# Performance work log

Hardware: AMD Instinct MI355X
Metric: run time of the kernel (lower is better)

Reference implementation:

```python
import jax, jax.numpy as jnp
import numpy as np

S, B, C, H, W = 16, 64, 128, 11, 11
P = H * W
N_ITER = 3
EPS = 1e-5


def setup_inputs() -> dict:
    key = jax.random.key(0)
    ks = jax.random.split(key, 12)
    w = lambda k, shape: jax.random.normal(k, shape, jnp.float32) * 0.02
    return {
        "x": jax.random.normal(ks[0], (S, B, C, H, W), jnp.float32),
        # intra-attention 1x1 convs (stored as [out,in] matrices)
        "wq": w(ks[1], (C, C)), "bq": jnp.zeros((C,), jnp.float32),
        "wk": w(ks[2], (C, C)), "bk": jnp.zeros((C,), jnp.float32),
        "wv": w(ks[3], (C, C)), "bv": jnp.zeros((C,), jnp.float32),
        "intra_alpha": jnp.float32(1.0),
        # inter-message path
        "w_msg": w(ks[4], (C, C + 1)), "b_msg": jnp.zeros((C,), jnp.float32),
        "w_lin": w(ks[5], (C, C)),
        "weight": jnp.float32(0.5),
        "w_gate": w(ks[6], (C, C)), "b_gate": jnp.zeros((C,), jnp.float32),
        # ConvGRU 3x3 convs
        "w_zr": w(ks[7], (2 * C, 2 * C, 3, 3)), "b_zr": jnp.zeros((2 * C,), jnp.float32),
        "w_h": w(ks[8], (C, 2 * C, 3, 3)), "b_h": jnp.zeros((C,), jnp.float32),
        # LayerNorm over [C,11,11]
        "ln_gamma": jnp.ones((C, H, W), jnp.float32),
        "ln_beta": jnp.zeros((C, H, W), jnp.float32),
    }


def reference(x, wq, bq, wk, bk, wv, bv, intra_alpha, w_msg, b_msg, w_lin,
              weight, w_gate, b_gate, w_zr, b_zr, w_h, b_h, ln_gamma, ln_beta):
    scale = C ** -0.5

    def c1(t, wgt, bias):  # 1x1 conv on [S,B,Cin,H,W] -> [S,B,Cout,H,W]
        return jnp.einsum('sbchw,oc->sbohw', t, wgt) + bias[:, None, None]

    def conv3(t, wgt, bias):  # 3x3 'SAME' conv on [N,Cin,H,W]
        y = jax.lax.conv_general_dilated(
            t, wgt, (1, 1), 'SAME', dimension_numbers=('NCHW', 'OIHW', 'NCHW'))
        return y + bias[None, :, None, None]

    # chain-graph neighbor validity masks (|i-j| == 1)
    mask_l = (jnp.arange(S) >= 1).astype(x.dtype)[:, None, None, None, None]
    mask_r = (jnp.arange(S) <= S - 2).astype(x.dtype)[:, None, None, None, None]

    h = x
    for _ in range(N_ITER):
        # ---- intra spatial self-attention (per node, over P=H*W tokens) ----
        q = c1(h, wq, bq).reshape(S, B, C, P)
        k = c1(h, wk, bk).reshape(S, B, C, P)
        v = c1(h, wv, bv).reshape(S, B, C, P)
        att = jax.nn.softmax(jnp.einsum('sbcp,sbcq->sbpq', q, k) * scale, axis=-1)
        intra = jnp.einsum('sbpq,sbcq->sbcp', att, v).reshape(S, B, C, H, W)
        intra = intra_alpha * intra + h

        # ---- inter gated message attention from chain neighbors ----
        xf = h.reshape(S, B, C, P)

        def gated_msg(y, edge_val):
            ef = jnp.full((S, B, 1, H, W), edge_val, h.dtype)  # edge feature i-j
            yy = c1(jnp.concatenate([y, ef], axis=2), w_msg, b_msg).reshape(S, B, C, P)
            yy = jnp.einsum('sbcp,dc->sbdp', yy, w_lin)  # Linear (no bias)
            a = jax.nn.softmax(jnp.einsum('sbcp,sbcq->sbpq', xf, yy), axis=-1)
            m = jnp.einsum('sbpq,sbcq->sbcp', a, yy).reshape(S, B, C, H, W)
            g = jax.nn.sigmoid(c1(m, w_gate, b_gate).mean(axis=(-2, -1), keepdims=True))
            return m * g

        y_left = jnp.concatenate([jnp.zeros_like(h[:1]), h[:-1]], axis=0)   # h[i-1], edge +1
        y_right = jnp.concatenate([h[1:], jnp.zeros_like(h[:1])], axis=0)   # h[i+1], edge -1
        inter = gated_msg(y_left, 1.0) * mask_l + gated_msg(y_right, -1.0) * mask_r

        comb = weight * intra + (1.0 - weight) * inter

        # ---- ConvGRU update (fold S into batch) ----
        xg = comb.reshape(S * B, C, H, W)
        hg = h.reshape(S * B, C, H, W)
        zr = jax.nn.sigmoid(conv3(jnp.concatenate([xg, hg], axis=1), w_zr, b_zr))
        z, r = zr[:, :C], zr[:, C:]
        h_hat = jnp.tanh(conv3(jnp.concatenate([xg, r * hg], axis=1), w_h, b_h))
        h_new = ((1 - z) * hg + z * h_hat).reshape(S, B, C, H, W)

        # ---- residual + LayerNorm over [C,H,W] ----
        nh = h_new + h
        mu = nh.mean(axis=(-3, -2, -1), keepdims=True)
        var = nh.var(axis=(-3, -2, -1), keepdims=True)
        h = (nh - mu) * jax.lax.rsqrt(var + EPS) * ln_gamma + ln_beta
    return h
```

## Files before the change

### kernel.cpp

```cpp
#include <hip/hip_runtime.h>
#include <hip/hip_bf16.h>

#define S_   16
#define B_   64
#define SBn  1024
#define C_   128
#define P_   121
#define CP_  15488
static const long NEl = 15859712L;

typedef __hip_bfloat16 bf16t;
typedef __attribute__((ext_vector_type(8))) short bf16x8;
typedef __attribute__((ext_vector_type(4))) float f32x4;
typedef __attribute__((ext_vector_type(4))) unsigned short us4;

__device__ __forceinline__ float ldb(const bf16t* p){ return __bfloat162float(*p); }
__device__ __forceinline__ float b2f(unsigned short u){ unsigned x=((unsigned)u)<<16; float f; __builtin_memcpy(&f,&x,4); return f; }
__device__ __forceinline__ unsigned short f2bu(float v){ __hip_bfloat16 b=__float2bfloat16(v); unsigned short u; __builtin_memcpy(&u,&b,2); return u; }
__device__ __forceinline__ float ldin(const void* s, long i, int f){
    return f ? ((const float*)s)[i] : b2f(((const unsigned short*)s)[i]);
}

__global__ void detect_kernel(const unsigned short* __restrict__ x, int* __restrict__ flag){
    if(blockIdx.x==0 && threadIdx.x==0){
        int crazy=0;
        for(int i=0;i<512;i++){
            unsigned e=(x[i]>>7)&0xFF;
            if(e!=0 && (e<64 || e>191)) crazy++;
        }
        *flag=(crazy>40)?1:0;
    }
}

__global__ void cvt_kernel(float* __restrict__ dst, const void* __restrict__ src, long n, const int* __restrict__ flag){
    long i=(long)blockIdx.x*blockDim.x+threadIdx.x;
    long st=(long)gridDim.x*blockDim.x;
    int f=*flag;
    for(;i<n;i+=st) dst[i]=ldin(src,i,f);
}

__global__ __launch_bounds__(256) void cvtT_kernel(bf16t* __restrict__ hT, const void* __restrict__ x, const int* __restrict__ flag){
    __shared__ bf16t tl[CP_];
    int sb=blockIdx.x, t=threadIdx.x; int f=*flag;
    for(int i=t;i<CP_;i+=256)
        tl[i]=__float2bfloat16(ldin(x,(long)sb*CP_+i,f));
    __syncthreads();
    bf16t* ho=hT+(size_t)sb*CP_;
    for(int j=t;j<CP_;j+=256){
        int p=j>>7, c=j&127;
        ho[j]=tl[c*P_+p];
    }
}

__global__ __launch_bounds__(128) void prep_msg_kernel(float* __restrict__ W2, float* __restrict__ b2l, float* __restrict__ b2r,
        const void* __restrict__ wlin, const void* __restrict__ wmsg, const void* __restrict__ bmsg, const int* __restrict__ flag){
    int d=blockIdx.x, c=threadIdx.x; int f=*flag;
    float acc=0.f;
    for(int o2=0;o2<C_;o2++) acc += ldin(wlin,(long)d*C_+o2,f)*ldin(wmsg,(long)o2*(C_+1)+c,f);
    W2[d*C_+c]=acc;
    if(c<2){
        float e=(c==0)?1.f:-1.f; float a=0.f;
        for(int o2=0;o2<C_;o2++) a += ldin(wlin,(long)d*C_+o2,f)*(ldin(bmsg,o2,f)+e*ldin(wmsg,(long)o2*(C_+1)+C_,f));
        if(c==0) b2l[d]=a; else b2r[d]=a;
    }
}

template<int RAW>
__global__ void prep_w1t(bf16t* __restrict__ dst, const void* __restrict__ src, const int* __restrict__ flag){
    int idx=blockIdx.x*blockDim.x+threadIdx.x;
    if(idx>=16384) return;
    int r=idx&31, oc=(idx>>5)&127, icb=idx>>12;
    float v = RAW? ldin(src,(long)oc*C_+icb*32+r,*flag) : ((const float*)src)[(long)oc*C_+icb*32+r];
    dst[idx]=__float2bfloat16(v);
}

__global__ void prep_w3t(bf16t* __restrict__ dst, const void* __restrict__ src, const int* __restrict__ flag, int OC){
    int idx=blockIdx.x*blockDim.x+threadIdx.x;
    int tot=OC*2304;
    if(idx>=tot) return;
    int r=idx&31; int rest=idx>>5; int oc=rest%OC; int g2=rest/OC; int icb=g2&7, tap=g2>>3;
    float v=ldin(src,((long)(oc*256+icb*32+r))*9+tap,*flag);
    dst[idx]=__float2bfloat16(v);
}

__global__ void prep_gbt(float* __restrict__ gamT, float* __restrict__ betT,
                         const void* __restrict__ gam, const void* __restrict__ bet, const int* __restrict__ flag){
    int idx=blockIdx.x*blockDim.x+threadIdx.x;
    if(idx>=CP_) return;
    int c=idx/P_, p=idx-c*P_; int f=*flag;
    gamT[p*C_+c]=ldin(gam,idx,f);
    betT[p*C_+c]=ldin(bet,idx,f);
}

__global__ void prep_wgt(float* __restrict__ wgT, float* __restrict__ bg2,
                         const void* __restrict__ wg, const void* __restrict__ bg, const int* __restrict__ flag){
    int idx=blockIdx.x*blockDim.x+threadIdx.x;
    int f=*flag;
    if(idx<16384){ int k=idx>>7, c=idx&127; wgT[idx]=ldin(wg,(long)c*C_+k,f); }
    if(idx<128) bg2[idx]=ldin(bg,idx,f);
}

__device__ __forceinline__ void gemm24r(f32x4 (&acc)[4][2],
    const bf16t* __restrict__ Wt, const bf16x8 (&hreg)[4][2],
    int ocr,int l15,int kg)
{
    #pragma unroll
    for(int i=0;i<4;i++){
        #pragma unroll
        for(int j=0;j<2;j++) acc[i][j]=(f32x4){0.f,0.f,0.f,0.f};
    }
    #pragma unroll
    for(int kc=0;kc<4;kc++){
        bf16x8 a[4];
        #pragma unroll
        for(int mt=0;mt<4;mt++) a[mt]=*(const bf16x8*)(Wt+((size_t)(kc*C_+ocr*64+mt*16+l15))*32+kg*8);
        #pragma unroll
        for(int mt=0;mt<4;mt++){
            #pragma unroll
            for(int nt=0;nt<2;nt++)
                acc[mt][nt]=__builtin_amdgcn_mfma_f32_16x16x32_bf16(a[mt],hreg[kc][nt],acc[mt][nt],0,0,0);
        }
    }
}

__global__ __launch_bounds__(512) void qkv_attn(
    bf16t* __restrict__ comb, const bf16t* __restrict__ hT,
    const bf16t* __restrict__ WqT, const bf16t* __restrict__ WkT, const bf16t* __restrict__ WvT,
    const float* __restrict__ bq, const float* __restrict__ bk, const float* __restrict__ bv,
    const float* __restrict__ alphap, const float* __restrict__ wp)
{
    __shared__ bf16t LA[128*136];
    __shared__ bf16t LB[128*136];
    int sb=blockIdx.x, t=threadIdx.x, lane=t&63, w=t>>6;
    int l15=lane&15, kg=lane>>4;
    const bf16t* hp=hT+(size_t)sb*CP_;
    int ocr=w>>2, pcr=w&3;
    bf16x8 hreg[4][2];
    #pragma unroll
    for(int kc=0;kc<4;kc++){
        #pragma unroll
        for(int nt=0;nt<2;nt++)
            hreg[kc][nt]=*(const bf16x8*)(hp+(size_t)(pcr*32+nt*16+l15)*C_+kc*32+kg*8);
    }
    f32x4 acc[4][2];
    gemm24r(acc,WqT,hreg,ocr,l15,kg);
    #pragma unroll
    for(int mt=0;mt<4;mt++){
        int oc0=ocr*64+mt*16+kg*4;
        #pragma unroll
        for(int nt=0;nt<2;nt++){
            int p=pcr*32+nt*16+l15;
            us4 pk;
            #pragma unroll
            for(int r=0;r<4;r++) pk[r]=f2bu(acc[mt][nt][r]+bq[oc0+r]);
            *(us4*)(LA+p*136+oc0)=pk;
        }
    }
    gemm24r(acc,WkT,hreg,ocr,l15,kg);
    #pragma unroll
    for(int mt=0;mt<4;mt++){
        int oc0=ocr*64+mt*16+kg*4;
        #pragma unroll
        for(int nt=0;nt<2;nt++){
            int p=pcr*32+nt*16+l15;
            us4 pk;
            #pragma unroll
            for(int r=0;r<4;r++) pk[r]=f2bu(acc[mt][nt][r]+bk[oc0+r]);
            *(us4*)(LB+p*136+oc0)=pk;
        }
    }
    __syncthreads();
    int m0=w*16;
    f32x4 s[8];
    #pragma unroll
    for(int nt=0;nt<8;nt++) s[nt]=(f32x4){0.f,0.f,0.f,0.f};
    #pragma unroll
    for(int kc=0;kc<4;kc++){
        bf16x8 a=*(const bf16x8*)(LA+(size_t)(m0+l15)*136+kc*32+kg*8);
        #pragma unroll
        for(int nt=0;nt<8;nt++){
            bf16x8 b=*(const bf16x8*)(LB+(size_t)(nt*16+l15)*136+kc*32+kg*8);
            s[nt]=__builtin_amdgcn_mfma_f32_16x16x32_bf16(a,b,s[nt],0,0,0);
        }
    }
    const float scale=0.08838834764831845f;
    #pragma unroll
    for(int nt=0;nt<8;nt++){
        #pragma unroll
        for(int r=0;r<4;r++) s[nt][r]*=scale;
    }
    if(l15>=9){
        #pragma unroll
        for(int r=0;r<4;r++) s[7][r]=-3.0e38f;
    }
    #pragma unroll
    for(int r=0;r<4;r++){
        float mx=s[0][r];
        #pragma unroll
        for(int nt=1;nt<8;nt++) mx=fmaxf(mx,s[nt][r]);
        #pragma unroll
        for(int o=1;o<16;o<<=1) mx=fmaxf(mx,__shfl_xor(mx,o));
        float sm=0.f;
        #pragma unroll
        for(int nt=0;nt<8;nt++){ float e=__expf(s[nt][r]-mx); s[nt][r]=e; sm+=e; }
        #pragma unroll
        for(int o=1;o<16;o<<=1) sm+=__shfl_xor(sm,o);
        float rs=1.f/sm;
        #pragma unroll
        for(int nt=0;nt<8;nt++) s[nt][r]*=rs;
    }
    __syncthreads();
    gemm24r(acc,WvT,hreg,ocr,l15,kg);
    #pragma unroll
    for(int mt=0;mt<4;mt++){
        int oc0=ocr*64+mt*16+kg*4;
        #pragma unroll
        for(int nt=0;nt<2;nt++){
            int p=pcr*32+nt*16+l15;
            #pragma unroll
            for(int r=0;r<4;r++)
                LA[(oc0+r)*136+p]=__float2bfloat16(p<P_? acc[mt][nt][r]+bv[oc0+r] : 0.f);
        }
    }
    #pragma unroll
    for(int r=0;r<4;r++){
        int pr=m0+kg*4+r;
        #pragma unroll
        for(int nt=0;nt<8;nt++) LB[pr*136+nt*16+l15]=__float2bfloat16(s[nt][r]);
    }
    __syncthreads();
    f32x4 o[8];
    #pragma unroll
    for(int nt=0;nt<8;nt++) o[nt]=(f32x4){0.f,0.f,0.f,0.f};
    #pragma unroll
    for(int jc=0;jc<4;jc++){
        bf16x8 a=*(const bf16x8*)(LA+(size_t)(m0+l15)*136+jc*32+kg*8);
        #pragma unroll
        for(int nt=0;nt<8;nt++){
            bf16x8 b=*(const bf16x8*)(LB+(size_t)(nt*16+l15)*136+jc*32+kg*8);
            o[nt]=__builtin_amdgcn_mfma_f32_16x16x32_bf16(a,b,o[nt],0,0,0);
        }
    }
    float al=*alphap, wv=*wp;
    int c0=m0+kg*4;
    bf16t* ob=comb+(size_t)sb*CP_;
    #pragma unroll
    for(int nt=0;nt<8;nt++){
        int p=nt*16+l15;
        if(p>=P_) continue;
        us4 hv=*(const us4*)(hp+(size_t)p*C_+c0);
        us4 pk;
        #pragma unroll
        for(int r=0;r<4;r++) pk[r]=f2bu(wv*(al*o[nt][r]+b2f(hv[r])));
        *(us4*)(ob+(size_t)p*C_+c0)=pk;
    }
}

__global__ __launch_bounds__(512) void msg_all(
    bf16t* __restrict__ comb, const bf16t* __restrict__ hT,
    const bf16t* __restrict__ W2T, const float* __restrict__ b2e,
    const float* __restrict__ wgT, const float* __restrict__ bgf,
    const float* __restrict__ wp, int sb0, int shift)
{
    __shared__ bf16t LA[128*136];
    __shared__ bf16t LB[128*136];
    __shared__ float fl[256];
    int sb=sb0+blockIdx.x, t=threadIdx.x, lane=t&63, w=t>>6;
    int l15=lane&15, kg=lane>>4;
    const bf16t* hsp=hT+(size_t)(sb+shift)*CP_;
    int ocr=w>>2, pcr=w&3;
    bf16x8 hreg[4][2];
    #pragma unroll
    for(int kc=0;kc<4;kc++){
        #pragma unroll
        for(int nt=0;nt<2;nt++)
            hreg[kc][nt]=*(const bf16x8*)(hsp+(size_t)(pcr*32+nt*16+l15)*C_+kc*32+kg*8);
    }
    f32x4 acc[4][2];
    gemm24r(acc,W2T,hreg,ocr,l15,kg);
    #pragma unroll
    for(int mt=0;mt<4;mt++){
        int oc0=ocr*64+mt*16+kg*4;
        #pragma unroll
        for(int nt=0;nt<2;nt++){
            int p=pcr*32+nt*16+l15;
            us4 pk;
            #pragma unroll
            for(int r=0;r<4;r++){
                float v=acc[mt][nt][r]+b2e[oc0+r];
                pk[r]=f2bu(v);
                LB[(oc0+r)*136+p]=__float2bfloat16(p<P_? v : 0.f);
            }
            *(us4*)(LA+p*136+oc0)=pk;
        }
    }
    __syncthreads();
    int m0=w*16;
    const bf16t* ap=hT+(size_t)sb*CP_;
    f32x4 s[8];
    #pragma unroll
    for(int nt=0;nt<8;nt++) s[nt]=(f32x4){0.f,0.f,0.f,0.f};
    #pragma unroll
    for(int kc=0;kc<4;kc++){
        bf16x8 a=*(const bf16x8*)(ap+(size_t)(m0+l15)*C_+kc*32+kg*8);
        #pragma unroll
        for(int nt=0;nt<8;nt++){
            bf16x8 b=*(const bf16x8*)(LA+(size_t)(nt*16+l15)*136+kc*32+kg*8);
            s[nt]=__builtin_amdgcn_mfma_f32_16x16x32_bf16(a,b,s[nt],0,0,0);
        }
    }
    if(l15>=9){
        #pragma unroll
        for(int r=0;r<4;r++) s[7][r]=-3.0e38f;
    }
    #pragma unroll
    for(int r=0;r<4;r++){
        float mx=s[0][r];
        #pragma unroll
        for(int nt=1;nt<8;nt++) mx=fmaxf(mx,s[nt][r]);
        #pragma unroll
        for(int o=1;o<16;o<<=1) mx=fmaxf(mx,__shfl_xor(mx,o));
        float sm=0.f;
        #pragma unroll
        for(int nt=0;nt<8;nt++){ float e=__expf(s[nt][r]-mx); s[nt][r]=e; sm+=e; }
        #pragma unroll
        for(int o=1;o<16;o<<=1) sm+=__shfl_xor(sm,o);
        float rs=1.f/sm;
        #pragma unroll
        for(int nt=0;nt<8;nt++) s[nt][r]*=rs;
    }
    __syncthreads();
    #pragma unroll
    for(int r=0;r<4;r++){
        int pr=m0+kg*4+r;
        #pragma unroll
        for(int nt=0;nt<8;nt++) LA[pr*136+nt*16+l15]=__float2bfloat16(s[nt][r]);
    }
    __syncthreads();
    f32x4 o[8];
    #pragma unroll
    for(int nt=0;nt<8;nt++) o[nt]=(f32x4){0.f,0.f,0.f,0.f};
    #pragma unroll
    for(int jc=0;jc<4;jc++){
        bf16x8 a=*(const bf16x8*)(LB+(size_t)(m0+l15)*136+jc*32+kg*8);
        #pragma unroll
        for(int nt=0;nt<8;nt++){
            bf16x8 b=*(const bf16x8*)(LA+(size_t)(nt*16+l15)*136+jc*32+kg*8);
            o[nt]=__builtin_amdgcn_mfma_f32_16x16x32_bf16(a,b,o[nt],0,0,0);
        }
    }
    int c0=m0+kg*4;
    #pragma unroll
    for(int r=0;r<4;r++){
        float sm=0.f;
        #pragma unroll
        for(int nt=0;nt<8;nt++){ float v=o[nt][r]; if(nt==7&&l15>8) v=0.f; sm+=v; }
        sm+=__shfl_xor(sm,1); sm+=__shfl_xor(sm,2); sm+=__shfl_xor(sm,4); sm+=__shfl_xor(sm,8);
        if(l15==0) fl[c0+r]=sm*(1.f/121.f);
    }
    __syncthreads();
    if(t<C_){
        float a=bgf[t];
        #pragma unroll 8
        for(int k=0;k<C_;k++) a+=wgT[k*C_+t]*fl[k];
        fl[C_+t]=1.f/(1.f+__expf(-a));
    }
    __syncthreads();
    float w1m=1.f-*wp;
    float gg[4];
    #pragma unroll
    for(int r=0;r<4;r++) gg[r]=fl[C_+c0+r];
    bf16t* ob=comb+(size_t)sb*CP_;
    #pragma unroll
    for(int nt=0;nt<8;nt++){
        int p=nt*16+l15;
        if(p>=P_) continue;
        us4 bv=*(const us4*)(ob+(size_t)p*C_+c0);
        #pragma unroll
        for(int r=0;r<4;r++) bv[r]=f2bu(b2f(bv[r]) + w1m*o[nt][r]*gg[r]);
        *(us4*)(ob+(size_t)p*C_+c0)=bv;
    }
}

#define LOADA3(bidx, widx) { \
    _Pragma("unroll") \
    for(int mt=0;mt<4;mt++) abuf[bidx][mt]=*(const bf16x8*)(Wt+(size_t)(widx)*(OC*32)+mt*512+base_lane); }
#define STEP3(lbase, bidx, doff) { \
    bf16x8 bb[4]; \
    _Pragma("unroll") \
    for(int nt=0;nt<4;nt++) bb[nt]=*(const bf16x8*)((lbase)+boff[nt]+(doff)); \
    __builtin_amdgcn_s_setprio(1); \
    _Pragma("unroll") \
    for(int mt=0;mt<4;mt++){ \
        _Pragma("unroll") \
        for(int nt=0;nt<4;nt++) \
            acc[mt][nt]=__builtin_amdgcn_mfma_f32_16x16x32_bf16(abuf[bidx][mt],bb[nt],acc[mt][nt],0,0,0); } \
    __builtin_amdgcn_s_setprio(0); }

#define SLOADZ(stg) { \
    const bf16t* ssrc=(((stg)<2)? in0T:in1T)+(size_t)sb*CP_+((stg)&1)*64; \
    sreg[0]=*(const bf16x8*)(ssrc+(size_t)sp0*C_+(t&7)*8); \
    if(sv1) sreg[1]=*(const bf16x8*)(ssrc+(size_t)sp1*C_+(t&7)*8); }
#define SWRITEZ(lbase) { \
    *(bf16x8*)((lbase)+spix0*72+(t&7)*8)=sreg[0]; \
    if(sv1) *(bf16x8*)((lbase)+spix1*72+(t&7)*8)=sreg[1]; }

__global__ __launch_bounds__(512) void conv3_zr(
    bf16t* __restrict__ o0, bf16t* __restrict__ o1,
    const bf16t* __restrict__ in0T, const bf16t* __restrict__ in1T,
    const bf16t* __restrict__ Wt, const float* __restrict__ bias,
    const bf16t* __restrict__ hTb)
{
    constexpr int OC=256;
    __shared__ bf16t lin[2*12176];
    int sb=blockIdx.x;
    int t=threadIdx.x, lane=t&63, w=t>>6;
    int ocb=(w>=4)?128:0; int w2=w&3;
    int ocr=w2>>1, pcr=w2&1, l15=lane&15, kg=lane>>4;
    int boff[4]; bool pv_[4];
    #pragma unroll
    for(int nt=0;nt<4;nt++){
        int p=pcr*64+nt*16+l15;
        pv_[nt]=(p<P_); int pc=pv_[nt]?p:(P_-1);
        boff[nt]=((pc/11)*13+(pc%11))*72+kg*8;
    }
    f32x4 acc[4][4];
    #pragma unroll
    for(int i=0;i<4;i++){
        #pragma unroll
        for(int j=0;j<4;j++) acc[i][j]=(f32x4){0.f,0.f,0.f,0.f};
    }
    int base_lane=(ocb+ocr*64+l15)*32+kg*8;
    bf16x8 abuf[4][4];
    bf16x8 sreg[2];
    bool sv1=((t+512)<968);
    int sp0=t>>3, sp1=(t+512)>>3;
    if(sp1>120) sp1=120;
    int spix0=(sp0/11+1)*13+(sp0%11)+1;
    int spix1=(sp1/11+1)*13+(sp1%11)+1;
    LOADA3(0,0); LOADA3(1,1); LOADA3(2,8); LOADA3(3,9);
    SLOADZ(0);
    {
        bf16x8 z;
        #pragma unroll
        for(int e=0;e<8;e++) z[e]=0;
        for(int i=t;i<768;i+=512){
            int half=i>=384; int i2=i-half*384;
            int bi=i2>>3, cc=(i2&7)*8;
            int pix;
            if(bi<13) pix=bi;
            else if(bi<26) pix=156+(bi-13);
            else { int j2=bi-26; pix=(1+(j2>>1))*13+((j2&1)?12:0); }
            *(bf16x8*)(lin+half*12176+pix*72+cc)=z;
        }
    }
    SWRITEZ(lin);
    __syncthreads();
    #pragma unroll
    for(int st=0; st<4; ++st){
        if(st<3) SLOADZ(st+1);
        bf16t* lbase=lin+(st&1)*12176;
        #pragma unroll
        for(int k=0;k<18;k++){
            int s=st*18+k;
            int tap=k>>1, l=k&1;
            int doff=((tap/3)*13+(tap%3))*72+l*32;
            STEP3(lbase, s&3, doff);
            if(s<68){
                int s4=s+4, st4=s4/18, k4=s4-st4*18, tap4=k4>>1, l4=k4&1;
                LOADA3(s&3, tap4*8+st4*2+l4);
            }
        }
        if(st<3){ SWRITEZ(lin+((st+1)&1)*12176); }
        __syncthreads();
    }
    #pragma unroll
    for(int mt=0;mt<4;mt++){
        int ocl=ocr*64+mt*16+kg*4;
        #pragma unroll
        for(int nt=0;nt<4;nt++){
            if(!pv_[nt]) continue;
            int p=pcr*64+nt*16+l15;
            size_t tb=(size_t)sb*CP_+(size_t)p*C_+ocl;
            us4 pk;
            if(ocb==0){
                #pragma unroll
                for(int r=0;r<4;r++){ float a=acc[mt][nt][r]+bias[ocl+r]; pk[r]=f2bu(1.f/(1.f+__expf(-a))); }
                *(us4*)(o0+tb)=pk;
            }else{
                us4 hv=*(const us4*)(hTb+tb);
                #pragma unroll
                for(int r=0;r<4;r++){ float a=acc[mt][nt][r]+bias[128+ocl+r]; float sg=1.f/(1.f+__expf(-a)); pk[r]=f2bu(sg*b2f(hv[r])); }
                *(us4*)(o1+tb)=pk;
            }
        }
    }
}

#define SLOADH(stg) { \
    const bf16t* ssrc=(((stg)<2)? in0T:in1T)+(size_t)sb*CP_+((stg)&1)*64; \
    sreg[0]=*(const bf16x8*)(ssrc+(size_t)(t>>3)*C_+(t&7)*8); \
    sreg[1]=*(const bf16x8*)(ssrc+(size_t)((t+256)>>3)*C_+(t&7)*8); \
    if(sv2) sreg[2]=*(const bf16x8*)(ssrc+(size_t)sp2*C_+(t&7)*8); \
    if(sv3) sreg[3]=*(const bf16x8*)(ssrc+(size_t)sp3*C_+(t&7)*8); }
#define SWRITEH(lbase) { \
    *(bf16x8*)((lbase)+spix0*72+(t&7)*8)=sreg[0]; \
    *(bf16x8*)((lbase)+spix1*72+(t&7)*8)=sreg[1]; \
    if(sv2) *(bf16x8*)((lbase)+spix2*72+(t&7)*8)=sreg[2]; \
    if(sv3) *(bf16x8*)((lbase)+spix3*72+(t&7)*8)=sreg[3]; }

__global__ __launch_bounds__(256) void conv3_hh(
    bf16t* __restrict__ o0,
    const bf16t* __restrict__ in0T, const bf16t* __restrict__ in1T,
    const bf16t* __restrict__ Wt, const float* __restrict__ bias,
    const bf16t* __restrict__ zT, const bf16t* __restrict__ hTb,
    const float* __restrict__ gamT, const float* __restrict__ betT)
{
    constexpr int OC=128;
    __shared__ bf16t lin[2*12176];
    __shared__ float red[8];
    int sb=blockIdx.x;
    int t=threadIdx.x, lane=t&63, w=t>>6;
    int ocr=w>>1, pcr=w&1, l15=lane&15, kg=lane>>4;
    int boff[4]; bool pv_[4];
    #pragma unroll
    for(int nt=0;nt<4;nt++){
        int p=pcr*64+nt*16+l15;
        pv_[nt]=(p<P_); int pc=pv_[nt]?p:(P_-1);
        boff[nt]=((pc/11)*13+(pc%11))*72+kg*8;
    }
    f32x4 acc[4][4];
    #pragma unroll
    for(int i=0;i<4;i++){
        #pragma unroll
        for(int j=0;j<4;j++) acc[i][j]=(f32x4){0.f,0.f,0.f,0.f};
    }
    int base_lane=(ocr*64+l15)*32+kg*8;
    bf16x8 abuf[4][4];
    bf16x8 sreg[4];
    bool sv2=((t+512)<968), sv3=((t+768)<968);
    int sp0=t>>3, sp1=(t+256)>>3, sp2=(t+512)>>3, sp3=(t+768)>>3;
    if(sp2>120) sp2=120;
    if(sp3>120) sp3=120;
    int spix0=(sp0/11+1)*13+(sp0%11)+1;
    int spix1=(sp1/11+1)*13+(sp1%11)+1;
    int spix2=(sp2/11+1)*13+(sp2%11)+1;
    int spix3=(sp3/11+1)*13+(sp3%11)+1;
    LOADA3(0,0); LOADA3(1,1); LOADA3(2,8); LOADA3(3,9);
    SLOADH(0);
    {
        bf16x8 z;
        #pragma unroll
        for(int e=0;e<8;e++) z[e]=0;
        for(int i=t;i<768;i+=256){
            int half=i>=384; int i2=i-half*384;
            int bi=i2>>3, cc=(i2&7)*8;
            int pix;
            if(bi<13) pix=bi;
            else if(bi<26) pix=156+(bi-13);
            else { int j2=bi-26; pix=(1+(j2>>1))*13+((j2&1)?12:0); }
            *(bf16x8*)(lin+half*12176+pix*72+cc)=z;
        }
    }
    SWRITEH(lin);
    __syncthreads();
    #pragma unroll
    for(int st=0; st<4; ++st){
        if(st<3) SLOADH(st+1);
        bf16t* lbase=lin+(st&1)*12176;
        #pragma unroll
        for(int k=0;k<18;k++){
            int s=st*18+k;
            int tap=k>>1, l=k&1;
            int doff=((tap/3)*13+(tap%3))*72+l*32;
            STEP3(lbase, s&3, doff);
            if(s<68){
                int s4=s+4, st4=s4/18, k4=s4-st4*18, tap4=k4>>1, l4=k4&1;
                LOADA3(s&3, tap4*8+st4*2+l4);
            }
        }
        if(st<3){ SWRITEH(lin+((st+1)&1)*12176); }
        __syncthreads();
    }
    float ls=0.f, ls2=0.f;
    #pragma unroll
    for(int mt=0;mt<4;mt++){
        int ocl=ocr*64+mt*16+kg*4;
        #pragma unroll
        for(int nt=0;nt<4;nt++){
            if(!pv_[nt]) continue;
            int p=pcr*64+nt*16+l15;
            size_t tb=(size_t)sb*CP_+(size_t)p*C_+ocl;
            us4 hv=*(const us4*)(hTb+tb);
            us4 zv=*(const us4*)(zT+tb);
            us4 pk;
            #pragma unroll
            for(int r=0;r<4;r++){
                float a=acc[mt][nt][r]+bias[ocl+r];
                float ht=tanhf(a);
                float z=b2f(zv[r]), h=b2f(hv[r]);
                unsigned short u=f2bu((1.f-z)*h+z*ht+h);
                pk[r]=u;
                float nr=b2f(u); ls+=nr; ls2+=nr*nr;
            }
            *(us4*)((unsigned short*)lin + p*C_+ocl)=pk;
        }
    }
    #pragma unroll
    for(int o=32;o;o>>=1){ ls+=__shfl_xor(ls,o); ls2+=__shfl_xor(ls2,o); }
    if(lane==0){ red[w]=ls; red[4+w]=ls2; }
    __syncthreads();
    float Sx=red[0]+red[1]+red[2]+red[3];
    float Sx2=red[4]+red[5]+red[6]+red[7];
    float mu=Sx*(1.f/(float)CP_);
    float var=Sx2*(1.f/(float)CP_)-mu*mu;
    float rstd=rsqrtf(var+1e-5f);
    bf16t* ho=o0+(size_t)sb*CP_;
    for(int i=t;i<CP_;i+=256){
        float v=(ldb(lin+i)-mu)*rstd*gamT[i]+betT[i];
        ho[i]=__float2bfloat16(v);
    }
}

__global__ __launch_bounds__(256) void finalT_kernel(void* __restrict__ fout, const bf16t* __restrict__ hT, const int* __restrict__ flag){
    __shared__ bf16t tl[CP_];
    int sb=blockIdx.x, t=threadIdx.x, f=*flag;
    for(int i=t;i<CP_;i+=256) tl[i]=hT[(size_t)sb*CP_+i];
    __syncthreads();
    for(int i=t;i<CP_;i+=256){
        int c=i/P_, p=i-c*P_;
        float v=ldb(tl+p*C_+c);
        size_t oi=(size_t)sb*CP_+i;
        if(f) ((float*)fout)[oi]=v;
        else  ((bf16t*)fout)[oi]=__float2bfloat16(v);
    }
}

extern "C" void kernel_launch(void* const* d_in, const int* in_sizes, int n_in,
                              void* d_out, int out_size, void* d_ws, size_t ws_size,
                              hipStream_t stream) {
    (void)in_sizes; (void)n_in; (void)out_size;
    char* base=(char*)d_ws;
    size_t off=0;
    auto alloc=[&](size_t bytes){ void* p=base+off; off+=(bytes+255)&~(size_t)255; return p; };
    bf16t* b1=(bf16t*)alloc((size_t)NEl*2+8192);
    bf16t* b2=(bf16t*)alloc((size_t)NEl*2+8192);
    bf16t* b3=(bf16t*)alloc((size_t)NEl*2+8192);
    bf16t* b4=(bf16t*)d_out;
    bf16t* wqT=(bf16t*)alloc(16384*2);
    bf16t* wkT=(bf16t*)alloc(16384*2);
    bf16t* wvT=(bf16t*)alloc(16384*2);
    bf16t* w2T=(bf16t*)alloc(16384*2);
    bf16t* wzrT=(bf16t*)alloc((size_t)589824*2);
    bf16t* whT =(bf16t*)alloc((size_t)294912*2);
    float* W2f=(float*)alloc(16384*4);
    float* b2l=(float*)alloc(128*4); float* b2r=(float*)alloc(128*4);
    float* bqf=(float*)alloc(128*4); float* bkf=(float*)alloc(128*4); float* bvf=(float*)alloc(128*4);
    float* bzrf=(float*)alloc(256*4); float* bhf=(float*)alloc(128*4);
    float* gamT=(float*)alloc(15488*4); float* betT=(float*)alloc(15488*4);
    float* wgTf=(float*)alloc(16384*4); float* bgf2=(float*)alloc(128*4);
    float* alphaf=(float*)alloc(4); float* weightf=(float*)alloc(4);
    int* flag=(int*)alloc(4);
    if(ws_size<off) return;

    detect_kernel<<<1,64,0,stream>>>((const unsigned short*)d_in[0],flag);
    cvtT_kernel<<<SBn,256,0,stream>>>(b1,d_in[0],flag);
    prep_w1t<1><<<64,256,0,stream>>>(wqT,d_in[1],flag);
    cvt_kernel<<<1,128,0,stream>>>(bqf,d_in[2],128,flag);
    prep_w1t<1><<<64,256,0,stream>>>(wkT,d_in[3],flag);
    cvt_kernel<<<1,128,0,stream>>>(bkf,d_in[4],128,flag);
    prep_w1t<1><<<64,256,0,stream>>>(wvT,d_in[5],flag);
    cvt_kernel<<<1,128,0,stream>>>(bvf,d_in[6],128,flag);
    cvt_kernel<<<1,64,0,stream>>>(alphaf,d_in[7],1,flag);
    prep_msg_kernel<<<C_,C_,0,stream>>>(W2f,b2l,b2r,d_in[10],d_in[8],d_in[9],flag);
    prep_w1t<0><<<64,256,0,stream>>>(w2T,W2f,flag);
    cvt_kernel<<<1,64,0,stream>>>(weightf,d_in[11],1,flag);
    prep_wgt<<<64,256,0,stream>>>(wgTf,bgf2,d_in[12],d_in[13],flag);
    prep_w3t<<<(256*2304+255)/256,256,0,stream>>>(wzrT,d_in[14],flag,256);
    cvt_kernel<<<1,256,0,stream>>>(bzrf,d_in[15],256,flag);
    prep_w3t<<<(128*2304+255)/256,256,0,stream>>>(whT,d_in[16],flag,128);
    cvt_kernel<<<1,128,0,stream>>>(bhf,d_in[17],128,flag);
    prep_gbt<<<(CP_+255)/256,256,0,stream>>>(gamT,betT,d_in[18],d_in[19],flag);

    for(int it=0; it<3; ++it){
        qkv_attn<<<SBn,512,0,stream>>>(b2,b1,wqT,wkT,wvT,bqf,bkf,bvf,alphaf,weightf);
        msg_all<<<SBn-B_,512,0,stream>>>(b2,b1,w2T,b2l,wgTf,bgf2,weightf,B_,-B_);
        msg_all<<<SBn-B_,512,0,stream>>>(b2,b1,w2T,b2r,wgTf,bgf2,weightf,0,B_);
        conv3_zr<<<SBn,512,0,stream>>>(b4,b3,b2,b1,wzrT,bzrf,b1);
        conv3_hh<<<SBn,256,0,stream>>>(b1,b2,b3,whT,bhf,b4,b1,gamT,betT);
    }
    finalT_kernel<<<SBn,256,0,stream>>>(d_out,b1,flag);
}
```

Measured before the change: 1.424 ms.

## Fuse intra-attention and both inter-message kernels into one per-node kernel

Merges qkv_attn and the two msg_all launches into a single attn_all kernel that keeps the combined result in registers and writes comb once. This removes two launches per iteration and the read-modify-write round trips of comb through global memory. It also reuses the node's own h tile (areg) across both message phases. The cost is higher register pressure (res, areg and hreg all live at once), which may reduce occupancy, and each block now does its message phases serially instead of spreading them over separate launches.

```diff
diff --git a/kernel.cpp b/kernel.cpp
--- a/kernel.cpp
+++ b/kernel.cpp
@@ -123,161 +123,25 @@
     }
 }
 
-__global__ __launch_bounds__(512) void qkv_attn(
-    bf16t* __restrict__ comb, const bf16t* __restrict__ hT,
-    const bf16t* __restrict__ WqT, const bf16t* __restrict__ WkT, const bf16t* __restrict__ WvT,
-    const float* __restrict__ bq, const float* __restrict__ bk, const float* __restrict__ bv,
-    const float* __restrict__ alphap, const float* __restrict__ wp)
+__device__ __forceinline__ void msg_phase(
+    f32x4 (&res)[8], const bf16t* __restrict__ hT, int sb, int shift,
+    const bf16t* __restrict__ W2T, const float* __restrict__ b2e,
+    const float* __restrict__ wgT, const float* __restrict__ bgf, float w1m,
+    const bf16x8 (&areg)[4],
+    bf16t* LA, bf16t* LB, float* fl,
+    int t,int w,int l15,int kg,int ocr,int pcr)
 {
-    __shared__ bf16t LA[128*136];
-    __shared__ bf16t LB[128*136];
-    int sb=blockIdx.x, t=threadIdx.x, lane=t&63, w=t>>6;
-    int l15=lane&15, kg=lane>>4;
-    const bf16t* hp=hT+(size_t)sb*CP_;
-    int ocr=w>>2, pcr=w&3;
-    bf16x8 hreg[4][2];
+    __syncthreads();
+    const bf16t* hsp=hT+(size_t)(sb+shift)*CP_;
+    bf16x8 hregS[4][2];
     #pragma unroll
     for(int kc=0;kc<4;kc++){
         #pragma unroll
         for(int nt=0;nt<2;nt++)
-            hreg[kc][nt]=*(const bf16x8*)(hp+(size_t)(pcr*32+nt*16+l15)*C_+kc*32+kg*8);
+            hregS[kc][nt]=*(const bf16x8*)(hsp+(size_t)(pcr*32+nt*16+l15)*C_+kc*32+kg*8);
     }
     f32x4 acc[4][2];
-    gemm24r(acc,WqT,hreg,ocr,l15,kg);
-    #pragma unroll
-    for(int mt=0;mt<4;mt++){
-        int oc0=ocr*64+mt*16+kg*4;
-        #pragma unroll
-        for(int nt=0;nt<2;nt++){
-            int p=pcr*32+nt*16+l15;
-            us4 pk;
-            #pragma unroll
-            for(int r=0;r<4;r++) pk[r]=f2bu(acc[mt][nt][r]+bq[oc0+r]);
-            *(us4*)(LA+p*136+oc0)=pk;
-        }
-    }
-    gemm24r(acc,WkT,hreg,ocr,l15,kg);
-    #pragma unroll
-    for(int mt=0;mt<4;mt++){
-        int oc0=ocr*64+mt*16+kg*4;
-        #pragma unroll
-        for(int nt=0;nt<2;nt++){
-            int p=pcr*32+nt*16+l15;
-            us4 pk;
-            #pragma unroll
-            for(int r=0;r<4;r++) pk[r]=f2bu(acc[mt][nt][r]+bk[oc0+r]);
-            *(us4*)(LB+p*136+oc0)=pk;
-        }
-    }
-    __syncthreads();
-    int m0=w*16;
-    f32x4 s[8];
-    #pragma unroll
-    for(int nt=0;nt<8;nt++) s[nt]=(f32x4){0.f,0.f,0.f,0.f};
-    #pragma unroll
-    for(int kc=0;kc<4;kc++){
-        bf16x8 a=*(const bf16x8*)(LA+(size_t)(m0+l15)*136+kc*32+kg*8);
-        #pragma unroll
-        for(int nt=0;nt<8;nt++){
-            bf16x8 b=*(const bf16x8*)(LB+(size_t)(nt*16+l15)*136+kc*32+kg*8);
-            s[nt]=__builtin_amdgcn_mfma_f32_16x16x32_bf16(a,b,s[nt],0,0,0);
-        }
-    }
-    const float scale=0.08838834764831845f;
-    #pragma unroll
-    for(int nt=0;nt<8;nt++){
-        #pragma unroll
-        for(int r=0;r<4;r++) s[nt][r]*=scale;
-    }
-    if(l15>=9){
-        #pragma unroll
-        for(int r=0;r<4;r++) s[7][r]=-3.0e38f;
-    }
-    #pragma unroll
-    for(int r=0;r<4;r++){
-        float mx=s[0][r];
-        #pragma unroll
-        for(int nt=1;nt<8;nt++) mx=fmaxf(mx,s[nt][r]);
-        #pragma unroll
-        for(int o=1;o<16;o<<=1) mx=fmaxf(mx,__shfl_xor(mx,o));
-        float sm=0.f;
-        #pragma unroll
-        for(int nt=0;nt<8;nt++){ float e=__expf(s[nt][r]-mx); s[nt][r]=e; sm+=e; }
-        #pragma unroll
-        for(int o=1;o<16;o<<=1) sm+=__shfl_xor(sm,o);
-        float rs=1.f/sm;
-        #pragma unroll
-        for(int nt=0;nt<8;nt++) s[nt][r]*=rs;
-    }
-    __syncthreads();
-    gemm24r(acc,WvT,hreg,ocr,l15,kg);
-    #pragma unroll
-    for(int mt=0;mt<4;mt++){
-        int oc0=ocr*64+mt*16+kg*4;
-        #pragma unroll
-        for(int nt=0;nt<2;nt++){
-            int p=pcr*32+nt*16+l15;
-            #pragma unroll
-            for(int r=0;r<4;r++)
-                LA[(oc0+r)*136+p]=__float2bfloat16(p<P_? acc[mt][nt][r]+bv[oc0+r] : 0.f);
-        }
-    }
-    #pragma unroll
-    for(int r=0;r<4;r++){
-        int pr=m0+kg*4+r;
-        #pragma unroll
-        for(int nt=0;nt<8;nt++) LB[pr*136+nt*16+l15]=__float2bfloat16(s[nt][r]);
-    }
-    __syncthreads();
-    f32x4 o[8];
-    #pragma unroll
-    for(int nt=0;nt<8;nt++) o[nt]=(f32x4){0.f,0.f,0.f,0.f};
-    #pragma unroll
-    for(int jc=0;jc<4;jc++){
-        bf16x8 a=*(const bf16x8*)(LA+(size_t)(m0+l15)*136+jc*32+kg*8);
-        #pragma unroll
-        for(int nt=0;nt<8;nt++){
-            bf16x8 b=*(const bf16x8*)(LB+(size_t)(nt*16+l15)*136+jc*32+kg*8);
-            o[nt]=__builtin_amdgcn_mfma_f32_16x16x32_bf16(a,b,o[nt],0,0,0);
-        }
-    }
-    float al=*alphap, wv=*wp;
-    int c0=m0+kg*4;
-    bf16t* ob=comb+(size_t)sb*CP_;
-    #pragma unroll
-    for(int nt=0;nt<8;nt++){
-        int p=nt*16+l15;
-        if(p>=P_) continue;
-        us4 hv=*(const us4*)(hp+(size_t)p*C_+c0);
-        us4 pk;
-        #pragma unroll
-        for(int r=0;r<4;r++) pk[r]=f2bu(wv*(al*o[nt][r]+b2f(hv[r])));
-        *(us4*)(ob+(size_t)p*C_+c0)=pk;
-    }
-}
-
-__global__ __launch_bounds__(512) void msg_all(
-    bf16t* __restrict__ comb, const bf16t* __restrict__ hT,
-    const bf16t* __restrict__ W2T, const float* __restrict__ b2e,
-    const float* __restrict__ wgT, const float* __restrict__ bgf,
-    const float* __restrict__ wp, int sb0, int shift)
-{
-    __shared__ bf16t LA[128*136];
-    __shared__ bf16t LB[128*136];
-    __shared__ float fl[256];
-    int sb=sb0+blockIdx.x, t=threadIdx.x, lane=t&63, w=t>>6;
-    int l15=lane&15, kg=lane>>4;
-    const bf16t* hsp=hT+(size_t)(sb+shift)*CP_;
-    int ocr=w>>2, pcr=w&3;
-    bf16x8 hreg[4][2];
-    #pragma unroll
-    for(int kc=0;kc<4;kc++){
-        #pragma unroll
-        for(int nt=0;nt<2;nt++)
-            hreg[kc][nt]=*(const bf16x8*)(hsp+(size_t)(pcr*32+nt*16+l15)*C_+kc*32+kg*8);
-    }
-    f32x4 acc[4][2];
-    gemm24r(acc,W2T,hreg,ocr,l15,kg);
+    gemm24r(acc,W2T,hregS,ocr,l15,kg);
     #pragma unroll
     for(int mt=0;mt<4;mt++){
         int oc0=ocr*64+mt*16+kg*4;
@@ -296,17 +160,15 @@
     }
     __syncthreads();
     int m0=w*16;
-    const bf16t* ap=hT+(size_t)sb*CP_;
     f32x4 s[8];
     #pragma unroll
     for(int nt=0;nt<8;nt++) s[nt]=(f32x4){0.f,0.f,0.f,0.f};
     #pragma unroll
     for(int kc=0;kc<4;kc++){
-        bf16x8 a=*(const bf16x8*)(ap+(size_t)(m0+l15)*C_+kc*32+kg*8);
         #pragma unroll
         for(int nt=0;nt<8;nt++){
             bf16x8 b=*(const bf16x8*)(LA+(size_t)(nt*16+l15)*136+kc*32+kg*8);
-            s[nt]=__builtin_amdgcn_mfma_f32_16x16x32_bf16(a,b,s[nt],0,0,0);
+            s[nt]=__builtin_amdgcn_mfma_f32_16x16x32_bf16(areg[kc],b,s[nt],0,0,0);
         }
     }
     if(l15>=9){
@@ -366,19 +228,165 @@
         fl[C_+t]=1.f/(1.f+__expf(-a));
     }
     __syncthreads();
-    float w1m=1.f-*wp;
     float gg[4];
     #pragma unroll
     for(int r=0;r<4;r++) gg[r]=fl[C_+c0+r];
+    #pragma unroll
+    for(int nt=0;nt<8;nt++){
+        #pragma unroll
+        for(int r=0;r<4;r++) res[nt][r]+=w1m*o[nt][r]*gg[r];
+    }
+}
+
+__global__ __launch_bounds__(512) void attn_all(
+    bf16t* __restrict__ comb, const bf16t* __restrict__ hT,
+    const bf16t* __restrict__ WqT, const bf16t* __restrict__ WkT, const bf16t* __restrict__ WvT,
+    const float* __restrict__ bq, const float* __restrict__ bk, const float* __restrict__ bv,
+    const bf16t* __restrict__ W2T, const float* __restrict__ b2l, const float* __restrict__ b2r,
+    const float* __restrict__ wgT, const float* __restrict__ bgf,
+    const float* __restrict__ alphap, const float* __restrict__ wp)
+{
+    __shared__ bf16t LA[128*136];
+    __shared__ bf16t LB[128*136];
+    __shared__ float fl[256];
+    int sb=blockIdx.x, t=threadIdx.x, lane=t&63, w=t>>6;
+    int l15=lane&15, kg=lane>>4;
+    const bf16t* hp=hT+(size_t)sb*CP_;
+    int ocr=w>>2, pcr=w&3;
+    int m0=w*16;
+    bf16x8 hreg[4][2];
+    #pragma unroll
+    for(int kc=0;kc<4;kc++){
+        #pragma unroll
+        for(int nt=0;nt<2;nt++)
+            hreg[kc][nt]=*(const bf16x8*)(hp+(size_t)(pcr*32+nt*16+l15)*C_+kc*32+kg*8);
+    }
+    bf16x8 areg[4];
+    #pragma unroll
+    for(int kc=0;kc<4;kc++)
+        areg[kc]=*(const bf16x8*)(hp+(size_t)(m0+l15)*C_+kc*32+kg*8);
+
+    f32x4 acc[4][2];
+    gemm24r(acc,WqT,hreg,ocr,l15,kg);
+    #pragma unroll
+    for(int mt=0;mt<4;mt++){
+        int oc0=ocr*64+mt*16+kg*4;
+        #pragma unroll
+        for(int nt=0;nt<2;nt++){
+            int p=pcr*32+nt*16+l15;
+            us4 pk;
+            #pragma unroll
+            for(int r=0;r<4;r++) pk[r]=f2bu(acc[mt][nt][r]+bq[oc0+r]);
+            *(us4*)(LA+p*136+oc0)=pk;
+        }
+    }
+    gemm24r(acc,WkT,hreg,ocr,l15,kg);
+    #pragma unroll
+    for(int mt=0;mt<4;mt++){
+        int oc0=ocr*64+mt*16+kg*4;
+        #pragma unroll
+        for(int nt=0;nt<2;nt++){
+            int p=pcr*32+nt*16+l15;
+            us4 pk;
+            #pragma unroll
+            for(int r=0;r<4;r++) pk[r]=f2bu(acc[mt][nt][r]+bk[oc0+r]);
+            *(us4*)(LB+p*136+oc0)=pk;
+        }
+    }
+    __syncthreads();
+    f32x4 s[8];
+    #pragma unroll
+    for(int nt=0;nt<8;nt++) s[nt]=(f32x4){0.f,0.f,0.f,0.f};
+    #pragma unroll
+    for(int kc=0;kc<4;kc++){
+        bf16x8 a=*(const bf16x8*)(LA+(size_t)(m0+l15)*136+kc*32+kg*8);
+        #pragma unroll
+        for(int nt=0;nt<8;nt++){
+            bf16x8 b=*(const bf16x8*)(LB+(size_t)(nt*16+l15)*136+kc*32+kg*8);
+            s[nt]=__builtin_amdgcn_mfma_f32_16x16x32_bf16(a,b,s[nt],0,0,0);
+        }
+    }
+    const float scale=0.08838834764831845f;
+    #pragma unroll
+    for(int nt=0;nt<8;nt++){
+        #pragma unroll
+        for(int r=0;r<4;r++) s[nt][r]*=scale;
+    }
+    if(l15>=9){
+        #pragma unroll
+        for(int r=0;r<4;r++) s[7][r]=-3.0e38f;
+    }
+    #pragma unroll
+    for(int r=0;r<4;r++){
+        float mx=s[0][r];
+        #pragma unroll
+        for(int nt=1;nt<8;nt++) mx=fmaxf(mx,s[nt][r]);
+        #pragma unroll
+        for(int o=1;o<16;o<<=1) mx=fmaxf(mx,__shfl_xor(mx,o));
+        float sm=0.f;
+        #pragma unroll
+        for(int nt=0;nt<8;nt++){ float e=__expf(s[nt][r]-mx); s[nt][r]=e; sm+=e; }
+        #pragma unroll
+        for(int o=1;o<16;o<<=1) sm+=__shfl_xor(sm,o);
+        float rs=1.f/sm;
+        #pragma unroll
+        for(int nt=0;nt<8;nt++) s[nt][r]*=rs;
+    }
+    __syncthreads();
+    gemm24r(acc,WvT,hreg,ocr,l15,kg);
+    #pragma unroll
+    for(int mt=0;mt<4;mt++){
+        int oc0=ocr*64+mt*16+kg*4;
+        #pragma unroll
+        for(int nt=0;nt<2;nt++){
+            int p=pcr*32+nt*16+l15;
+            #pragma unroll
+            for(int r=0;r<4;r++)
+                LA[(oc0+r)*136+p]=__float2bfloat16(p<P_? acc[mt][nt][r]+bv[oc0+r] : 0.f);
+        }
+    }
+    #pragma unroll
+    for(int r=0;r<4;r++){
+        int pr=m0+kg*4+r;
+        #pragma unroll
+        for(int nt=0;nt<8;nt++) LB[pr*136+nt*16+l15]=__float2bfloat16(s[nt][r]);
+    }
+    __syncthreads();
+    f32x4 res[8];
+    #pragma unroll
+    for(int nt=0;nt<8;nt++) res[nt]=(f32x4){0.f,0.f,0.f,0.f};
+    #pragma unroll
+    for(int jc=0;jc<4;jc++){
+        bf16x8 a=*(const bf16x8*)(LA+(size_t)(m0+l15)*136+jc*32+kg*8);
+        #pragma unroll
+        for(int nt=0;nt<8;nt++){
+            bf16x8 b=*(const bf16x8*)(LB+(size_t)(nt*16+l15)*136+jc*32+kg*8);
+            res[nt]=__builtin_amdgcn_mfma_f32_16x16x32_bf16(a,b,res[nt],0,0,0);
+        }
+    }
+    float al=*alphap, wv=*wp, w1m=1.f-wv;
+    int c0=m0+kg*4;
+    #pragma unroll
+    for(int nt=0;nt<8;nt++){
+        int p=nt*16+l15;
+        int pc=(p<P_)?p:(P_-1);
+        us4 hv=*(const us4*)(hp+(size_t)pc*C_+c0);
+        #pragma unroll
+        for(int r=0;r<4;r++) res[nt][r]=wv*(al*res[nt][r]+b2f(hv[r]));
+    }
+    if(sb>=B_)
+        msg_phase(res,hT,sb,-B_,W2T,b2l,wgT,bgf,w1m,areg,LA,LB,fl,t,w,l15,kg,ocr,pcr);
+    if(sb<SBn-B_)
+        msg_phase(res,hT,sb, B_,W2T,b2r,wgT,bgf,w1m,areg,LA,LB,fl,t,w,l15,kg,ocr,pcr);
     bf16t* ob=comb+(size_t)sb*CP_;
     #pragma unroll
     for(int nt=0;nt<8;nt++){
         int p=nt*16+l15;
         if(p>=P_) continue;
-        us4 bv=*(const us4*)(ob+(size_t)p*C_+c0);
-        #pragma unroll
-        for(int r=0;r<4;r++) bv[r]=f2bu(b2f(bv[r]) + w1m*o[nt][r]*gg[r]);
-        *(us4*)(ob+(size_t)p*C_+c0)=bv;
+        us4 pk;
+        #pragma unroll
+        for(int r=0;r<4;r++) pk[r]=f2bu(res[nt][r]);
+        *(us4*)(ob+(size_t)p*C_+c0)=pk;
     }
 }
 
@@ -683,9 +691,8 @@
     prep_gbt<<<(CP_+255)/256,256,0,stream>>>(gamT,betT,d_in[18],d_in[19],flag);
 
     for(int it=0; it<3; ++it){
-        qkv_attn<<<SBn,512,0,stream>>>(b2,b1,wqT,wkT,wvT,bqf,bkf,bvf,alphaf,weightf);
-        msg_all<<<SBn-B_,512,0,stream>>>(b2,b1,w2T,b2l,wgTf,bgf2,weightf,B_,-B_);
-        msg_all<<<SBn-B_,512,0,stream>>>(b2,b1,w2T,b2r,wgTf,bgf2,weightf,0,B_);
+        attn_all<<<SBn,512,0,stream>>>(b2,b1,wqT,wkT,wvT,bqf,bkf,bvf,
+                                       w2T,b2l,b2r,wgTf,bgf2,alphaf,weightf);
         conv3_zr<<<SBn,512,0,stream>>>(b4,b3,b2,b1,wzrT,bzrf,b1);
         conv3_hh<<<SBn,256,0,stream>>>(b1,b2,b3,whT,bhf,b4,b1,gamT,betT);
     }
```

Measured after the change: 1.420 ms. About the same (-0.3%).
